# Kernel optimization log

Hardware: AMD Instinct MI355X
Metric: run time of the kernel (lower is better)

The kernel has to match this reference:

```python
import jax, jax.numpy as jnp
import numpy as np
from jax import lax

N, E, F, H, B = 16384, 262144, 32, 128, 16
DI, DS, DC, DTR = 256, 16, 4, 8   # Mamba: d_inner=expand*H, d_state, d_conv, dt_rank=ceil(H/16)
NS, NC = 512, 8                   # num_stations, num line colors
EPS = 1e-5


def _forward(node_features, edge_index, batch, W_in, b_in, W_g1, b_g1, W_g2, b_g2,
             W_inproj, conv_w, conv_b, W_xproj, W_dt, b_dt, A_log, D_p, W_out,
             gamma, beta, Wc, bc, Wh, bh, Wt, bt, Wp1, bp1, Wp2, bp2, Wd, bd, Ws, bs):
    def gcn(x, W, b):
        # GCNConv with self-loops and symmetric normalization
        loops = jnp.arange(N)
        s = jnp.concatenate([edge_index[0], loops])
        d = jnp.concatenate([edge_index[1], loops])
        deg = jax.ops.segment_sum(jnp.ones(s.shape[0], x.dtype), d, num_segments=N)
        dinv = jnp.where(deg > 0, lax.rsqrt(deg), 0.0)
        xw = x @ W
        msg = xw[s] * (dinv[s] * dinv[d])[:, None]
        return jax.ops.segment_sum(msg, d, num_segments=N) + b

    h = jax.nn.relu(node_features @ W_in + b_in)
    h = jax.nn.relu(gcn(h, W_g1, b_g1))
    h_gnn = jax.nn.relu(gcn(h, W_g2, b_g2))

    # --- Mamba block over the node sequence (batch dim of 1, seq_len = N) ---
    xz = h_gnn @ W_inproj                      # (N, 2*DI)
    x, z = xz[:, :DI], xz[:, DI:]
    xp = jnp.pad(x, ((DC - 1, 0), (0, 0)))     # causal depthwise conv1d
    xc = conv_b + sum(xp[k:k + N] * conv_w[:, k] for k in range(DC))
    x = jax.nn.silu(xc)
    dbl = x @ W_xproj                          # (N, DTR + 2*DS)
    dt = jax.nn.softplus(dbl[:, :DTR] @ W_dt + b_dt)   # (N, DI)
    Bm = dbl[:, DTR:DTR + DS]                  # (N, DS)
    Cm = dbl[:, DTR + DS:]                     # (N, DS)
    A = -jnp.exp(A_log)                        # (DI, DS)
    dA = jnp.exp(dt[:, :, None] * A[None])     # (N, DI, DS)
    dBx = dt[:, :, None] * Bm[:, None, :] * x[:, :, None]

    def step(hst, t):
        dA_t, dBx_t, C_t = t
        hst = dA_t * hst + dBx_t               # (DI, DS)
        return hst, hst @ C_t                  # (DI,)

    _, ys = lax.scan(step, jnp.zeros((DI, DS), x.dtype), (dA, dBx, Cm))
    y = (ys + D_p * x) * jax.nn.silu(z)
    h_mamba = y @ W_out                        # (N, H)

    # residual + LayerNorm
    hh = h_gnn + h_mamba
    mu = hh.mean(-1, keepdims=True)
    var = ((hh - mu) ** 2).mean(-1, keepdims=True)
    h_final = (hh - mu) * lax.rsqrt(var + EPS) * gamma + beta

    # global_mean_pool per graph
    counts = jax.ops.segment_sum(jnp.ones(N, h_final.dtype), batch, num_segments=B)
    ge = jax.ops.segment_sum(h_final, batch, num_segments=B) / jnp.maximum(counts, 1.0)[:, None]

    # critic + all policy heads, concatenated: [1,4,3,NS,NS,NS,NC]
    return jnp.concatenate([ge @ Wc + bc, ge @ Wh + bh, ge @ Wt + bt,
                            ge @ Wp1 + bp1, ge @ Wp2 + bp2, ge @ Wd + bd,
                            ge @ Ws + bs], axis=-1)


def setup_inputs() -> dict:
    key = jax.random.key(0)
    ks = list(jax.random.split(key, 20))
    p = lambda i, shape, s=0.02: jax.random.normal(ks[i], shape, jnp.float32) * s
    return dict(
        node_features=jax.random.normal(ks[0], (N, F), jnp.float32),
        edge_index=jax.random.randint(ks[1], (2, E), 0, N),
        batch=jnp.sort(jax.random.randint(ks[2], (N,), 0, B)),
        W_in=p(3, (F, H)), b_in=jnp.zeros((H,), jnp.float32),
        W_g1=p(4, (H, H)), b_g1=jnp.zeros((H,), jnp.float32),
        W_g2=p(5, (H, H)), b_g2=jnp.zeros((H,), jnp.float32),
        W_inproj=p(6, (H, 2 * DI)),
        conv_w=p(7, (DI, DC)), conv_b=jnp.zeros((DI,), jnp.float32),
        W_xproj=p(8, (DI, DTR + 2 * DS)),
        W_dt=p(9, (DTR, DI)), b_dt=jnp.full((DI,), -4.0, jnp.float32),
        A_log=jnp.log(jnp.broadcast_to(jnp.arange(1.0, DS + 1.0, dtype=jnp.float32), (DI, DS))),
        D_p=jnp.ones((DI,), jnp.float32),
        W_out=p(10, (DI, H)),
        gamma=jnp.ones((H,), jnp.float32), beta=jnp.zeros((H,), jnp.float32),
        Wc=p(11, (H, 1)), bc=jnp.zeros((1,), jnp.float32),
        Wh=p(12, (H, 4)), bh=jnp.zeros((4,), jnp.float32),
        Wt=p(13, (H, 3)), bt=jnp.zeros((3,), jnp.float32),
        Wp1=p(14, (H, NS)), bp1=jnp.zeros((NS,), jnp.float32),
        Wp2=p(15, (H, NS)), bp2=jnp.zeros((NS,), jnp.float32),
        Wd=p(16, (H, NS)), bd=jnp.zeros((NS,), jnp.float32),
        Ws=p(17, (H, NC)), bs=jnp.zeros((NC,), jnp.float32),
    )


def reference(node_features, edge_index, batch, W_in, b_in, W_g1, b_g1, W_g2, b_g2,
              W_inproj, conv_w, conv_b, W_xproj, W_dt, b_dt, A_log, D_p, W_out,
              gamma, beta, Wc, bc, Wh, bh, Wt, bt, Wp1, bp1, Wp2, bp2, Wd, bd, Ws, bs):
    return _forward(node_features, edge_index, batch, W_in, b_in, W_g1, b_g1, W_g2, b_g2,
                    W_inproj, conv_w, conv_b, W_xproj, W_dt, b_dt, A_log, D_p, W_out,
                    gamma, beta, Wc, bc, Wh, bh, Wt, bt, Wp1, bp1, Wp2, bp2, Wd, bd, Ws, bs)
```

## Files before the change

kernel.cpp:

```cpp
#include <hip/hip_runtime.h>
#include <math.h>

#define NN 16384
#define EE 262144
#define FF 32
#define HH 128
#define BB 16
#define DI 256
#define DS 16
#define DC 4
#define DTR 8
#define OUTW 1552
#define NCH 256
#define CHLEN 64

__device__ __forceinline__ float siluf(float v) { return v / (1.f + __expf(-v)); }
__device__ __forceinline__ float softplusf(float v) {
    return fmaxf(v, 0.f) + __logf(1.f + __expf(-fabsf(v)));
}

__global__ void zero_kernel(int* __restrict__ cnt, float* __restrict__ ge,
                            int* __restrict__ counts) {
    int idx = blockIdx.x * blockDim.x + threadIdx.x;
    if (idx < NN) cnt[idx] = 0;
    if (idx < BB * HH) ge[idx] = 0.f;
    if (idx < BB) counts[idx] = 0;
}

__global__ void deg_kernel(const int* __restrict__ dst, int* __restrict__ cnt) {
    int e = blockIdx.x * blockDim.x + threadIdx.x;
    if (e < EE) atomicAdd(&cnt[dst[e]], 1);
}

__global__ __launch_bounds__(1024) void prefix_kernel(const int* __restrict__ cnt,
                                                      int* __restrict__ rowptr,
                                                      int* __restrict__ cursor,
                                                      float* __restrict__ dinv) {
    __shared__ int part[1024];
    int tid = threadIdx.x;
    int4 c4[4];
#pragma unroll
    for (int j = 0; j < 4; j++) c4[j] = ((const int4*)cnt)[tid * 4 + j];
    int v[16] = {c4[0].x, c4[0].y, c4[0].z, c4[0].w, c4[1].x, c4[1].y, c4[1].z, c4[1].w,
                 c4[2].x, c4[2].y, c4[2].z, c4[2].w, c4[3].x, c4[3].y, c4[3].z, c4[3].w};
    int s = 0;
#pragma unroll
    for (int j = 0; j < 16; j++) s += v[j];
    part[tid] = s;
    __syncthreads();
    for (int off = 1; off < 1024; off <<= 1) {
        int t = (tid >= off) ? part[tid - off] : 0;
        __syncthreads();
        part[tid] += t;
        __syncthreads();
    }
    int running = part[tid] - s;
    int rp[16];
    float dv[16];
#pragma unroll
    for (int j = 0; j < 16; j++) {
        rp[j] = running;
        running += v[j];
        dv[j] = rsqrtf((float)(v[j] + 1));
    }
#pragma unroll
    for (int j = 0; j < 4; j++) {
        int4 r4; r4.x = rp[j*4]; r4.y = rp[j*4+1]; r4.z = rp[j*4+2]; r4.w = rp[j*4+3];
        ((int4*)rowptr)[tid * 4 + j] = r4;
        ((int4*)cursor)[tid * 4 + j] = r4;
        float4 d4; d4.x = dv[j*4]; d4.y = dv[j*4+1]; d4.z = dv[j*4+2]; d4.w = dv[j*4+3];
        ((float4*)dinv)[tid * 4 + j] = d4;
    }
    if (tid == 1023) rowptr[NN] = part[1023];
}

__global__ void scatter_kernel(const int* __restrict__ src, const int* __restrict__ dst,
                               int* __restrict__ cursor, int* __restrict__ col) {
    int e = blockIdx.x * blockDim.x + threadIdx.x;
    if (e < EE) {
        int d = dst[e];
        int pos = atomicAdd(&cursor[d], 1);
        col[pos] = src[e];
    }
}

__global__ __launch_bounds__(256) void gemm_k(const float* __restrict__ A,
                                              const float* __restrict__ B,
                                              const float* __restrict__ bias,
                                              float* __restrict__ C,
                                              int M, int Nn, int K, int act) {
    __shared__ float As[16][68];
    __shared__ float Bs[16][68];
    int tid = threadIdx.x;
    int m0 = blockIdx.y * 64;
    int n0 = blockIdx.x * 64;
    int ty = tid >> 4, tx = tid & 15;
    float acc[4][4] = {{0.f}};
    for (int k0 = 0; k0 < K; k0 += 16) {
#pragma unroll
        for (int l = 0; l < 4; l++) {
            int idx = tid + l * 256;
            int i = idx >> 4, j = idx & 15;
            As[j][i] = A[(size_t)(m0 + i) * K + k0 + j];
        }
#pragma unroll
        for (int l = 0; l < 4; l++) {
            int idx = tid + l * 256;
            int i = idx >> 6, j = idx & 63;
            int n = n0 + j;
            Bs[i][j] = (n < Nn) ? B[(size_t)(k0 + i) * Nn + n] : 0.f;
        }
        __syncthreads();
#pragma unroll
        for (int kk = 0; kk < 16; kk++) {
            float4 a4 = *(const float4*)&As[kk][ty * 4];
            float4 b4 = *(const float4*)&Bs[kk][tx * 4];
            float av[4] = {a4.x, a4.y, a4.z, a4.w};
            float bv[4] = {b4.x, b4.y, b4.z, b4.w};
#pragma unroll
            for (int r = 0; r < 4; r++)
#pragma unroll
                for (int c = 0; c < 4; c++) acc[r][c] = fmaf(av[r], bv[c], acc[r][c]);
        }
        __syncthreads();
    }
    int nb = n0 + tx * 4;
    if (nb < Nn) {
        float4 bi4 = {0.f, 0.f, 0.f, 0.f};
        if (bias) bi4 = *(const float4*)&bias[nb];
#pragma unroll
        for (int r = 0; r < 4; r++) {
            int m = m0 + ty * 4 + r;
            float4 v;
            v.x = acc[r][0] + bi4.x; v.y = acc[r][1] + bi4.y;
            v.z = acc[r][2] + bi4.z; v.w = acc[r][3] + bi4.w;
            if (act == 1) {
                v.x = fmaxf(v.x, 0.f); v.y = fmaxf(v.y, 0.f);
                v.z = fmaxf(v.z, 0.f); v.w = fmaxf(v.w, 0.f);
            }
            *(float4*)&C[(size_t)m * Nn + nb] = v;
        }
    }
}

union SMemIn {
    struct { float Ns[64][33]; float Ws[32][132]; } s1;
    float Bs[16][68];
};

__global__ __launch_bounds__(256) void gemm_in_g1(const float* __restrict__ nf,
                                                  const float* __restrict__ W_in,
                                                  const float* __restrict__ b_in,
                                                  const float* __restrict__ W_g1,
                                                  float* __restrict__ out) {
    __shared__ SMemIn sm;
    __shared__ float Hs[128][68];
    int tid = threadIdx.x;
    int m0 = blockIdx.y * 64;
    int n0 = blockIdx.x * 64;
    int ty = tid >> 4, tx = tid & 15;
#pragma unroll
    for (int l = 0; l < 2; l++) {
        int q = tid + l * 256;
        int r = q >> 3, c4 = (q & 7) * 4;
        *(float4*)&sm.s1.Ns[r][c4] = *(const float4*)&nf[(size_t)(m0 + r) * FF + c4];
    }
#pragma unroll
    for (int l = 0; l < 4; l++) {
        int q = tid + l * 256;
        int r = q >> 5, c4 = (q & 31) * 4;
        *(float4*)&sm.s1.Ws[r][c4] = *(const float4*)&W_in[(size_t)r * HH + c4];
    }
    __syncthreads();
    {
        float4 b0 = *(const float4*)&b_in[tx * 4];
        float4 b1 = *(const float4*)&b_in[64 + tx * 4];
        float hacc[4][8];
#pragma unroll
        for (int r = 0; r < 4; r++) {
            hacc[r][0] = b0.x; hacc[r][1] = b0.y; hacc[r][2] = b0.z; hacc[r][3] = b0.w;
            hacc[r][4] = b1.x; hacc[r][5] = b1.y; hacc[r][6] = b1.z; hacc[r][7] = b1.w;
        }
#pragma unroll
        for (int k = 0; k < FF; k++) {
            float av[4];
#pragma unroll
            for (int r = 0; r < 4; r++) av[r] = sm.s1.Ns[ty * 4 + r][k];
            float wv[8];
#pragma unroll
            for (int c = 0; c < 4; c++) {
                wv[c]     = sm.s1.Ws[k][tx * 4 + c];
                wv[c + 4] = sm.s1.Ws[k][64 + tx * 4 + c];
            }
#pragma unroll
            for (int r = 0; r < 4; r++)
#pragma unroll
                for (int c = 0; c < 8; c++) hacc[r][c] = fmaf(av[r], wv[c], hacc[r][c]);
        }
#pragma unroll
        for (int r = 0; r < 4; r++)
#pragma unroll
            for (int c = 0; c < 4; c++) {
                Hs[tx * 4 + c][ty * 4 + r]      = fmaxf(hacc[r][c], 0.f);
                Hs[64 + tx * 4 + c][ty * 4 + r] = fmaxf(hacc[r][c + 4], 0.f);
            }
    }
    __syncthreads();
    float acc[4][4] = {{0.f}};
    for (int k0 = 0; k0 < HH; k0 += 16) {
        *(float4*)&sm.Bs[tid >> 4][(tid & 15) * 4] =
            *(const float4*)&W_g1[(size_t)(k0 + (tid >> 4)) * HH + n0 + (tid & 15) * 4];
        __syncthreads();
#pragma unroll
        for (int kk = 0; kk < 16; kk++) {
            float4 a4 = *(const float4*)&Hs[k0 + kk][ty * 4];
            float4 b4 = *(const float4*)&sm.Bs[kk][tx * 4];
            float av[4] = {a4.x, a4.y, a4.z, a4.w};
            float bv[4] = {b4.x, b4.y, b4.z, b4.w};
#pragma unroll
            for (int r = 0; r < 4; r++)
#pragma unroll
                for (int c = 0; c < 4; c++) acc[r][c] = fmaf(av[r], bv[c], acc[r][c]);
        }
        __syncthreads();
    }
#pragma unroll
    for (int r = 0; r < 4; r++) {
        int m = m0 + ty * 4 + r;
        float4 v;
        v.x = acc[r][0]; v.y = acc[r][1]; v.z = acc[r][2]; v.w = acc[r][3];
        *(float4*)&out[(size_t)m * HH + n0 + tx * 4] = v;
    }
}

__global__ __launch_bounds__(512, 4) void gemm_big512_t(const float* __restrict__ A,
                                                        const float* __restrict__ B,
                                                        float* __restrict__ CT,
                                                        int M, int Nn, int K) {
    __shared__ float As[16][132];
    __shared__ float Bs[16][132];
    int tid = threadIdx.x;
    int m0 = blockIdx.y * 128;
    int n0 = blockIdx.x * 128;
    int ty = tid >> 4;
    int tx = tid & 15;
    float acc[4][8] = {{0.f}};
    for (int k0 = 0; k0 < K; k0 += 16) {
        {
            int m = tid >> 2;
            int kc = (tid & 3) * 4;
            float4 a = *(const float4*)&A[(size_t)(m0 + m) * K + k0 + kc];
            As[kc + 0][m] = a.x; As[kc + 1][m] = a.y;
            As[kc + 2][m] = a.z; As[kc + 3][m] = a.w;
        }
        {
            int krow = tid >> 5;
            int c4 = (tid & 31) * 4;
            *(float4*)&Bs[krow][c4] = *(const float4*)&B[(size_t)(k0 + krow) * Nn + n0 + c4];
        }
        __syncthreads();
#pragma unroll
        for (int kk = 0; kk < 16; kk++) {
            float4 a4 = *(const float4*)&As[kk][ty * 4];
            float4 b0 = *(const float4*)&Bs[kk][tx * 4];
            float4 b1 = *(const float4*)&Bs[kk][64 + tx * 4];
            float av[4] = {a4.x, a4.y, a4.z, a4.w};
            float bv[8] = {b0.x, b0.y, b0.z, b0.w, b1.x, b1.y, b1.z, b1.w};
#pragma unroll
            for (int r = 0; r < 4; r++)
#pragma unroll
                for (int c = 0; c < 8; c++) acc[r][c] = fmaf(av[r], bv[c], acc[r][c]);
        }
        __syncthreads();
    }
#pragma unroll
    for (int cc = 0; cc < 4; cc++) {
        float4 v;
        v.x = acc[0][cc]; v.y = acc[1][cc]; v.z = acc[2][cc]; v.w = acc[3][cc];
        *(float4*)&CT[(size_t)(n0 + tx * 4 + cc) * NN + m0 + ty * 4] = v;
        float4 u;
        u.x = acc[0][cc + 4]; u.y = acc[1][cc + 4]; u.z = acc[2][cc + 4]; u.w = acc[3][cc + 4];
        *(float4*)&CT[(size_t)(n0 + 64 + tx * 4 + cc) * NN + m0 + ty * 4] = u;
    }
}

__global__ __launch_bounds__(256) void gemm_xz_dblt(const float* __restrict__ xzt,
                                                    const float* __restrict__ B,
                                                    const float* __restrict__ cw,
                                                    const float* __restrict__ cb,
                                                    float* __restrict__ xst,
                                                    float* __restrict__ dblt) {
    __shared__ float As[16][68];
    __shared__ float Bs[16][68];
    __shared__ float Raw[16][72];
    __shared__ float Ct[64][41];
    int tid = threadIdx.x;
    int m0 = blockIdx.x * 64;
    int ty = tid >> 4, tx = tid & 15;
    float acc[4][4] = {{0.f}};
    for (int k0 = 0; k0 < DI; k0 += 16) {
#pragma unroll
        for (int l = 0; l < 2; l++) {
            int idx = tid + l * 256;
            if (idx < 272) {
                int kk = idx / 17, j = idx % 17;
                int tcol = m0 - 4 + j * 4;
                float4 v;
                if (tcol >= 0) v = *(const float4*)&xzt[(size_t)(k0 + kk) * NN + tcol];
                else { v.x = 0.f; v.y = 0.f; v.z = 0.f; v.w = 0.f; }
                *(float4*)&Raw[kk][j * 4] = v;
            }
        }
#pragma unroll
        for (int l = 0; l < 4; l++) {
            int idx = tid + l * 256;
            int i2 = idx >> 6, j2 = idx & 63;
            Bs[i2][j2] = (j2 < 40) ? B[(size_t)(k0 + i2) * 40 + j2] : 0.f;
        }
        __syncthreads();
#pragma unroll
        for (int l = 0; l < 4; l++) {
            int kk = (tid >> 6) + l * 4;
            int i = tid & 63;
            int d = k0 + kk;
            float w0 = cw[d * DC + 0], w1 = cw[d * DC + 1];
            float w2 = cw[d * DC + 2], w3 = cw[d * DC + 3];
            float v = siluf(cb[d] + w0 * Raw[kk][i + 1] + w1 * Raw[kk][i + 2]
                                  + w2 * Raw[kk][i + 3] + w3 * Raw[kk][i + 4]);
            As[kk][i] = v;
            xst[(size_t)d * NN + m0 + i] = v;
        }
        __syncthreads();
#pragma unroll
        for (int kk = 0; kk < 16; kk++) {
            float4 a4 = *(const float4*)&As[kk][ty * 4];
            float4 b4 = *(const float4*)&Bs[kk][tx * 4];
            float av[4] = {a4.x, a4.y, a4.z, a4.w};
            float bv[4] = {b4.x, b4.y, b4.z, b4.w};
#pragma unroll
            for (int r = 0; r < 4; r++)
#pragma unroll
                for (int c = 0; c < 4; c++) acc[r][c] = fmaf(av[r], bv[c], acc[r][c]);
        }
        __syncthreads();
    }
    if (tx * 4 < 40) {
#pragma unroll
        for (int r = 0; r < 4; r++) {
            int m = ty * 4 + r;
            Ct[m][tx * 4 + 0] = acc[r][0];
            Ct[m][tx * 4 + 1] = acc[r][1];
            Ct[m][tx * 4 + 2] = acc[r][2];
            Ct[m][tx * 4 + 3] = acc[r][3];
        }
    }
    __syncthreads();
#pragma unroll
    for (int l = 0; l < 10; l++) {
        int idx = tid + l * 256;
        int n = idx >> 6, m = idx & 63;
        dblt[(size_t)n * NN + m0 + m] = Ct[m][n];
    }
}

__global__ __launch_bounds__(256) void gemm_at_ln_pool(const float* __restrict__ AT,
                                                       const float* __restrict__ B,
                                                       const float* __restrict__ hg,
                                                       const float* __restrict__ gamma,
                                                       const float* __restrict__ beta,
                                                       const int* __restrict__ batch,
                                                       float* __restrict__ ge,
                                                       int* __restrict__ counts) {
    __shared__ float As[16][36];
    __shared__ float Bs[16][132];
    __shared__ float lnb[32][132];
    __shared__ int gb[32];
    int tid = threadIdx.x;
    int m0 = blockIdx.x * 32;
    int ty = tid >> 4, tx = tid & 15;
    float acc[2][8] = {{0.f}};
    for (int k0 = 0; k0 < 256; k0 += 16) {
        {
            int idx = tid * 2;
            int kk = idx >> 5, i = idx & 31;
            As[kk][i] = AT[(size_t)(k0 + kk) * NN + m0 + i];
            As[kk][i + 1] = AT[(size_t)(k0 + kk) * NN + m0 + i + 1];
        }
        {
            int krow = tid >> 4;
            int c8 = (tid & 15) * 8;
            const float* bp = &B[(size_t)(k0 + krow) * HH + c8];
            *(float4*)&Bs[krow][c8] = *(const float4*)bp;
            *(float4*)&Bs[krow][c8 + 4] = *(const float4*)(bp + 4);
        }
        __syncthreads();
#pragma unroll
        for (int kk = 0; kk < 16; kk++) {
            float a0 = As[kk][ty * 2];
            float a1 = As[kk][ty * 2 + 1];
            float4 b0 = *(const float4*)&Bs[kk][tx * 4];
            float4 b1 = *(const float4*)&Bs[kk][64 + tx * 4];
            float bv[8] = {b0.x, b0.y, b0.z, b0.w, b1.x, b1.y, b1.z, b1.w};
#pragma unroll
            for (int c = 0; c < 8; c++) {
                acc[0][c] = fmaf(a0, bv[c], acc[0][c]);
                acc[1][c] = fmaf(a1, bv[c], acc[1][c]);
            }
        }
        __syncthreads();
    }
    if (tid < 32) gb[tid] = batch[m0 + tid];
    float4 g0 = *(const float4*)&gamma[tx * 4];
    float4 g1 = *(const float4*)&gamma[64 + tx * 4];
    float4 be0 = *(const float4*)&beta[tx * 4];
    float4 be1 = *(const float4*)&beta[64 + tx * 4];
    float gv[8] = {g0.x, g0.y, g0.z, g0.w, g1.x, g1.y, g1.z, g1.w};
    float bv[8] = {be0.x, be0.y, be0.z, be0.w, be1.x, be1.y, be1.z, be1.w};
#pragma unroll
    for (int r = 0; r < 2; r++) {
        int m = m0 + ty * 2 + r;
        float4 h0 = *(const float4*)&hg[(size_t)m * HH + tx * 4];
        float4 h1 = *(const float4*)&hg[(size_t)m * HH + 64 + tx * 4];
        float v[8] = {acc[r][0] + h0.x, acc[r][1] + h0.y, acc[r][2] + h0.z, acc[r][3] + h0.w,
                      acc[r][4] + h1.x, acc[r][5] + h1.y, acc[r][6] + h1.z, acc[r][7] + h1.w};
        float sum = 0.f;
#pragma unroll
        for (int c = 0; c < 8; c++) sum += v[c];
        sum += __shfl_xor(sum, 1); sum += __shfl_xor(sum, 2);
        sum += __shfl_xor(sum, 4); sum += __shfl_xor(sum, 8);
        float mu = sum * (1.f / 128.f);
        float vs = 0.f;
#pragma unroll
        for (int c = 0; c < 8; c++) { float dd = v[c] - mu; vs += dd * dd; }
        vs += __shfl_xor(vs, 1); vs += __shfl_xor(vs, 2);
        vs += __shfl_xor(vs, 4); vs += __shfl_xor(vs, 8);
        float inv = rsqrtf(vs * (1.f / 128.f) + 1e-5f);
        int lr = ty * 2 + r;
        float4 o0, o1;
        o0.x = (v[0] - mu) * inv * gv[0] + bv[0];
        o0.y = (v[1] - mu) * inv * gv[1] + bv[1];
        o0.z = (v[2] - mu) * inv * gv[2] + bv[2];
        o0.w = (v[3] - mu) * inv * gv[3] + bv[3];
        o1.x = (v[4] - mu) * inv * gv[4] + bv[4];
        o1.y = (v[5] - mu) * inv * gv[5] + bv[5];
        o1.z = (v[6] - mu) * inv * gv[6] + bv[6];
        o1.w = (v[7] - mu) * inv * gv[7] + bv[7];
        *(float4*)&lnb[lr][tx * 4] = o0;
        *(float4*)&lnb[lr][64 + tx * 4] = o1;
    }
    __syncthreads();
    if (tid < HH) {
        int f = tid;
        int gcur = gb[0];
        float acc2 = 0.f;
        int cnt = 0;
#pragma unroll 4
        for (int i = 0; i < 32; i++) {
            int g = gb[i];
            if (g != gcur) {
                atomicAdd(&ge[gcur * HH + f], acc2);
                if (f == 0) atomicAdd(&counts[gcur], cnt);
                acc2 = 0.f; cnt = 0; gcur = g;
            }
            acc2 += lnb[i][f];
            cnt++;
        }
        atomicAdd(&ge[gcur * HH + f], acc2);
        if (f == 0) atomicAdd(&counts[gcur], cnt);
    }
}

__global__ __launch_bounds__(256) void gcn_gather4(const float* __restrict__ xw,
                                                   const int* __restrict__ rowptr,
                                                   const int* __restrict__ col,
                                                   const float* __restrict__ dinv,
                                                   const float* __restrict__ b,
                                                   float* __restrict__ out) {
    int tid = threadIdx.x;
    int sub = tid & 31;
    int n = blockIdx.x * 8 + (tid >> 5);
    float dn = dinv[n];
    const float4* xw4 = (const float4*)xw;
    float4 a = xw4[(size_t)n * 32 + sub];
    float ws = dn * dn;
    float4 acc;
    acc.x = a.x * ws; acc.y = a.y * ws; acc.z = a.z * ws; acc.w = a.w * ws;
    int beg = rowptr[n], end = rowptr[n + 1];
    int e = beg;
    for (; e + 4 <= end; e += 4) {
        int s0 = col[e], s1 = col[e + 1], s2 = col[e + 2], s3 = col[e + 3];
        float w0 = dinv[s0] * dn, w1 = dinv[s1] * dn;
        float w2 = dinv[s2] * dn, w3 = dinv[s3] * dn;
        float4 v0 = xw4[(size_t)s0 * 32 + sub];
        float4 v1 = xw4[(size_t)s1 * 32 + sub];
        float4 v2 = xw4[(size_t)s2 * 32 + sub];
        float4 v3 = xw4[(size_t)s3 * 32 + sub];
        acc.x = fmaf(v0.x, w0, acc.x); acc.y = fmaf(v0.y, w0, acc.y);
        acc.z = fmaf(v0.z, w0, acc.z); acc.w = fmaf(v0.w, w0, acc.w);
        acc.x = fmaf(v1.x, w1, acc.x); acc.y = fmaf(v1.y, w1, acc.y);
        acc.z = fmaf(v1.z, w1, acc.z); acc.w = fmaf(v1.w, w1, acc.w);
        acc.x = fmaf(v2.x, w2, acc.x); acc.y = fmaf(v2.y, w2, acc.y);
        acc.z = fmaf(v2.z, w2, acc.z); acc.w = fmaf(v2.w, w2, acc.w);
        acc.x = fmaf(v3.x, w3, acc.x); acc.y = fmaf(v3.y, w3, acc.y);
        acc.z = fmaf(v3.z, w3, acc.z); acc.w = fmaf(v3.w, w3, acc.w);
    }
    for (; e < end; e++) {
        int s0 = col[e];
        float w0 = dinv[s0] * dn;
        float4 v0 = xw4[(size_t)s0 * 32 + sub];
        acc.x = fmaf(v0.x, w0, acc.x); acc.y = fmaf(v0.y, w0, acc.y);
        acc.z = fmaf(v0.z, w0, acc.z); acc.w = fmaf(v0.w, w0, acc.w);
    }
    float4 b4 = ((const float4*)b)[sub];
    acc.x = fmaxf(acc.x + b4.x, 0.f);
    acc.y = fmaxf(acc.y + b4.y, 0.f);
    acc.z = fmaxf(acc.z + b4.z, 0.f);
    acc.w = fmaxf(acc.w + b4.w, 0.f);
    ((float4*)out)[(size_t)n * 32 + sub] = acc;
}

__global__ __launch_bounds__(256, 6) void scan_phase1(const float* __restrict__ xst,
                                                      const float* __restrict__ dblt,
                                                      const float* __restrict__ A_log,
                                                      const float* __restrict__ W_dt,
                                                      const float* __restrict__ b_dt,
                                                      float* __restrict__ chkP,
                                                      float* __restrict__ chkH) {
    __shared__ float Td[32][68];
    __shared__ float Tx[32][68];
    __shared__ float Bs[16][68];
    __shared__ float D8[8][68];
    int tid = threadIdx.x;
    int wave = tid >> 6, lane = tid & 63;
    int sg = lane & 7, dl = lane >> 3;
    int dblk = blockIdx.x, chunk = blockIdx.y;
    int t0 = chunk * CHLEN;
    int dloc = wave * 8 + dl;
    int d = dblk * 32 + dloc;
    int s0 = 2 * sg;
#pragma unroll
    for (int p = 0; p < 2; p++) {
        int linear = tid + p * 256;
        int row = linear >> 4, c4 = (linear & 15) * 4;
        *(float4*)&Tx[row][c4] = *(const float4*)&xst[(size_t)(dblk * 32 + row) * NN + t0 + c4];
    }
    if (tid < 128) {
        int r = tid >> 4, c4 = (tid & 15) * 4;
        *(float4*)&D8[r][c4] = *(const float4*)&dblt[(size_t)r * NN + t0 + c4];
    }
    {
        int s = tid >> 4, c4 = (tid & 15) * 4;
        *(float4*)&Bs[s][c4] = *(const float4*)&dblt[(size_t)(8 + s) * NN + t0 + c4];
    }
    float A0 = -expf(A_log[d * DS + s0]);
    float A1 = -expf(A_log[d * DS + s0 + 1]);
    __syncthreads();
    {
        int row = tid >> 3;
        int tb = (tid & 7) * 8;
        int dd = dblk * 32 + row;
        float bd = b_dt[dd];
        float wv[8];
#pragma unroll
        for (int j = 0; j < 8; j++) wv[j] = W_dt[j * DI + dd];
#pragma unroll
        for (int j = 0; j < 8; j++) {
            int t = tb + j;
            float acc = bd;
#pragma unroll
            for (int k = 0; k < 8; k++) acc = fmaf(D8[k][t], wv[k], acc);
            Td[row][t] = softplusf(acc);
        }
    }
    __syncthreads();
    float h0 = 0.f, h1 = 0.f, P0 = 1.f, P1 = 1.f;
    for (int i = 0; i < CHLEN; i += 4) {
        float4 d4 = *(const float4*)&Td[dloc][i];
        float4 x4 = *(const float4*)&Tx[dloc][i];
        float4 b04 = *(const float4*)&Bs[s0][i];
        float4 b14 = *(const float4*)&Bs[s0 + 1][i];
#define P1S(U) { float dtv = d4.U; float a0 = __expf(dtv * A0); float a1 = __expf(dtv * A1); \
        float dx = dtv * x4.U; h0 = fmaf(a0, h0, dx * b04.U); h1 = fmaf(a1, h1, dx * b14.U); \
        P0 *= a0; P1 *= a1; }
        P1S(x) P1S(y) P1S(z) P1S(w)
#undef P1S
    }
    int idx = chunk * 4096 + d * DS + s0;
    float2 vP; vP.x = P0; vP.y = P1;
    float2 vH; vH.x = h0; vH.y = h1;
    *(float2*)(chkP + idx) = vP;
    *(float2*)(chkH + idx) = vH;
}

__global__ void scan_phase2(const float* __restrict__ chkP, const float* __restrict__ chkH,
                            float* __restrict__ init) {
    int idx = blockIdx.x * blockDim.x + threadIdx.x;
    float h = 0.f;
    for (int c0 = 0; c0 < NCH; c0 += 8) {
        float p[8], q[8];
#pragma unroll
        for (int j = 0; j < 8; j++) {
            p[j] = chkP[(c0 + j) * 4096 + idx];
            q[j] = chkH[(c0 + j) * 4096 + idx];
        }
#pragma unroll
        for (int j = 0; j < 8; j++) {
            init[(c0 + j) * 4096 + idx] = h;
            h = fmaf(p[j], h, q[j]);
        }
    }
}

__global__ __launch_bounds__(256, 6) void scan_phase3(const float* __restrict__ xst,
                                                      const float* __restrict__ dblt,
                                                      const float* __restrict__ A_log,
                                                      const float* __restrict__ W_dt,
                                                      const float* __restrict__ b_dt,
                                                      const float* __restrict__ init,
                                                      const float* __restrict__ D_p,
                                                      const float* __restrict__ xzt,
                                                      float* __restrict__ yt) {
    __shared__ float Td[32][68];
    __shared__ float Tx[32][68];
    __shared__ float Bs[16][68];
    __shared__ float CsD8[16][68];
    int tid = threadIdx.x;
    int wave = tid >> 6, lane = tid & 63;
    int sg = lane & 7, dl = lane >> 3;
    int dblk = blockIdx.x, chunk = blockIdx.y;
    int t0 = chunk * CHLEN;
    int dloc = wave * 8 + dl;
    int d = dblk * 32 + dloc;
    int s0 = 2 * sg;
#pragma unroll
    for (int p = 0; p < 2; p++) {
        int linear = tid + p * 256;
        int row = linear >> 4, c4 = (linear & 15) * 4;
        *(float4*)&Tx[row][c4] = *(const float4*)&xst[(size_t)(dblk * 32 + row) * NN + t0 + c4];
    }
    if (tid < 128) {
        int r = tid >> 4, c4 = (tid & 15) * 4;
        *(float4*)&CsD8[r][c4] = *(const float4*)&dblt[(size_t)r * NN + t0 + c4];
    }
    {
        int s = tid >> 4, c4 = (tid & 15) * 4;
        *(float4*)&Bs[s][c4] = *(const float4*)&dblt[(size_t)(8 + s) * NN + t0 + c4];
    }
    float A0 = -expf(A_log[d * DS + s0]);
    float A1 = -expf(A_log[d * DS + s0 + 1]);
    float Dd = D_p[d];
    float2 ini = *(const float2*)(init + chunk * 4096 + d * DS + s0);
    float h0 = ini.x, h1 = ini.y;
    __syncthreads();
    {
        int row = tid >> 3;
        int tb = (tid & 7) * 8;
        int dd = dblk * 32 + row;
        float bd = b_dt[dd];
        float wv[8];
#pragma unroll
        for (int j = 0; j < 8; j++) wv[j] = W_dt[j * DI + dd];
#pragma unroll
        for (int j = 0; j < 8; j++) {
            int t = tb + j;
            float acc = bd;
#pragma unroll
            for (int k = 0; k < 8; k++) acc = fmaf(CsD8[k][t], wv[k], acc);
            Td[row][t] = softplusf(acc);
        }
    }
    __syncthreads();
    {
        int s = tid >> 4, c4 = (tid & 15) * 4;
        *(float4*)&CsD8[s][c4] = *(const float4*)&dblt[(size_t)(24 + s) * NN + t0 + c4];
    }
    float szv[8];
#pragma unroll
    for (int r = 0; r < 8; r++)
        szv[r] = siluf(xzt[(size_t)(256 + dblk * 32 + wave * 8 + r) * NN + t0 + lane]);
    __syncthreads();
    for (int i = 0; i < CHLEN; i += 4) {
        float4 d4 = *(const float4*)&Td[dloc][i];
        float4 x4 = *(const float4*)&Tx[dloc][i];
        float4 b04 = *(const float4*)&Bs[s0][i];
        float4 b14 = *(const float4*)&Bs[s0 + 1][i];
        float4 c04 = *(const float4*)&CsD8[s0][i];
        float4 c14 = *(const float4*)&CsD8[s0 + 1][i];
        float4 yv;
#define P3S(U) { float dtv = d4.U; float a0 = __expf(dtv * A0); float a1 = __expf(dtv * A1); \
        float dx = dtv * x4.U; h0 = fmaf(a0, h0, dx * b04.U); h1 = fmaf(a1, h1, dx * b14.U); \
        float c = fmaf(h1, c14.U, h0 * c04.U); \
        c += __shfl_xor(c, 1); c += __shfl_xor(c, 2); c += __shfl_xor(c, 4); \
        yv.U = c + Dd * x4.U; }
        P3S(x) P3S(y) P3S(z) P3S(w)
#undef P3S
        if (sg == 0) *(float4*)&Td[dloc][i] = yv;
    }
#pragma unroll
    for (int r = 0; r < 8; r++) {
        int row = wave * 8 + r;
        yt[(size_t)(dblk * 32 + row) * NN + t0 + lane] = Td[row][lane] * szv[r];
    }
}

__global__ void heads_kernel(const float* __restrict__ ge, const int* __restrict__ counts,
                             const float* Wc, const float* bc, const float* Wh, const float* bh,
                             const float* Wt, const float* bt, const float* Wp1, const float* bp1,
                             const float* Wp2, const float* bp2, const float* Wd, const float* bd,
                             const float* Ws, const float* bs, float* __restrict__ out) {
    int col = blockIdx.x * blockDim.x + threadIdx.x;
    int b = blockIdx.y;
    if (col >= OUTW) return;
    const float* W; const float* bi; int lc, w;
    if (col < 1)         { W = Wc;  bi = bc;  lc = col;        w = 1; }
    else if (col < 5)    { W = Wh;  bi = bh;  lc = col - 1;    w = 4; }
    else if (col < 8)    { W = Wt;  bi = bt;  lc = col - 5;    w = 3; }
    else if (col < 520)  { W = Wp1; bi = bp1; lc = col - 8;    w = 512; }
    else if (col < 1032) { W = Wp2; bi = bp2; lc = col - 520;  w = 512; }
    else if (col < 1544) { W = Wd;  bi = bd;  lc = col - 1032; w = 512; }
    else                 { W = Ws;  bi = bs;  lc = col - 1544; w = 8; }
    float scale = 1.f / fmaxf((float)counts[b], 1.f);
    float dot = 0.f;
#pragma unroll 8
    for (int f = 0; f < HH; f++) dot = fmaf(ge[b * HH + f], W[f * w + lc], dot);
    out[(size_t)b * OUTW + col] = bi[lc] + scale * dot;
}

extern "C" void kernel_launch(void* const* d_in, const int* in_sizes, int n_in,
                              void* d_out, int out_size, void* d_ws, size_t ws_size,
                              hipStream_t stream) {
    const float* nf      = (const float*)d_in[0];
    const int*   ei      = (const int*)d_in[1];
    const int*   batch   = (const int*)d_in[2];
    const float* W_in    = (const float*)d_in[3];
    const float* b_in    = (const float*)d_in[4];
    const float* W_g1    = (const float*)d_in[5];
    const float* b_g1    = (const float*)d_in[6];
    const float* W_g2    = (const float*)d_in[7];
    const float* b_g2    = (const float*)d_in[8];
    const float* W_inproj= (const float*)d_in[9];
    const float* conv_w  = (const float*)d_in[10];
    const float* conv_b  = (const float*)d_in[11];
    const float* W_xproj = (const float*)d_in[12];
    const float* W_dt    = (const float*)d_in[13];
    const float* b_dt    = (const float*)d_in[14];
    const float* A_log   = (const float*)d_in[15];
    const float* D_p     = (const float*)d_in[16];
    const float* W_out   = (const float*)d_in[17];
    const float* gamma   = (const float*)d_in[18];
    const float* beta    = (const float*)d_in[19];
    const float* Wc = (const float*)d_in[20]; const float* bc = (const float*)d_in[21];
    const float* Wh = (const float*)d_in[22]; const float* bh = (const float*)d_in[23];
    const float* Wt = (const float*)d_in[24]; const float* bt = (const float*)d_in[25];
    const float* Wp1= (const float*)d_in[26]; const float* bp1= (const float*)d_in[27];
    const float* Wp2= (const float*)d_in[28]; const float* bp2= (const float*)d_in[29];
    const float* Wd = (const float*)d_in[30]; const float* bd = (const float*)d_in[31];
    const float* Ws = (const float*)d_in[32]; const float* bs = (const float*)d_in[33];

    const int* e_src = ei;
    const int* e_dst = ei + EE;

    float* w = (float*)d_ws;
    size_t o = 0;
    float* F0   = w + o; o += (size_t)NN * HH;
    float* F1   = w + o; o += (size_t)NN * HH;
    float* F2   = w + o; o += (size_t)NN * HH;
    float* XZT  = w + o; o += (size_t)NN * 512;
    float* YT   = XZT;
    float* XST  = w + o; o += (size_t)NN * DI;
    float* DBLT = w + o; o += (size_t)NN * 40;
    float* GE   = w + o; o += BB * HH;
    float* DINV = w + o; o += NN;
    int* ip = (int*)(w + o);
    int* CNT    = ip; ip += NN;
    int* ROWPTR = ip; ip += NN + 1;
    int* CURSOR = ip; ip += NN;
    int* COL    = ip; ip += EE;
    int* COUNTS = ip; ip += BB;

    float* CHP  = F0;
    float* CHH  = F0 + (size_t)NCH * 4096;
    float* INI  = F1;

    zero_kernel<<<(NN + 255) / 256, 256, 0, stream>>>(CNT, GE, COUNTS);

    deg_kernel<<<EE / 256, 256, 0, stream>>>(e_dst, CNT);
    prefix_kernel<<<1, 1024, 0, stream>>>(CNT, ROWPTR, CURSOR, DINV);
    scatter_kernel<<<EE / 256, 256, 0, stream>>>(e_src, e_dst, CURSOR, COL);

    gemm_in_g1<<<dim3(2, NN / 64), 256, 0, stream>>>(nf, W_in, b_in, W_g1, F1);
    gcn_gather4<<<NN / 8, 256, 0, stream>>>(F1, ROWPTR, COL, DINV, b_g1, F0);
    gemm_k<<<dim3(2, NN / 64), 256, 0, stream>>>(F0, W_g2, nullptr, F1, NN, HH, HH, 0);
    gcn_gather4<<<NN / 8, 256, 0, stream>>>(F1, ROWPTR, COL, DINV, b_g2, F2);

    gemm_big512_t<<<dim3(4, NN / 128), 512, 0, stream>>>(F2, W_inproj, XZT, NN, 512, HH);
    gemm_xz_dblt<<<NN / 64, 256, 0, stream>>>(XZT, W_xproj, conv_w, conv_b, XST, DBLT);

    scan_phase1<<<dim3(8, NCH), 256, 0, stream>>>(XST, DBLT, A_log, W_dt, b_dt, CHP, CHH);
    scan_phase2<<<16, 256, 0, stream>>>(CHP, CHH, INI);
    scan_phase3<<<dim3(8, NCH), 256, 0, stream>>>(XST, DBLT, A_log, W_dt, b_dt, INI, D_p, XZT, YT);

    gemm_at_ln_pool<<<NN / 32, 256, 0, stream>>>(YT, W_out, F2, gamma, beta, batch, GE, COUNTS);

    heads_kernel<<<dim3((OUTW + 127) / 128, BB), 128, 0, stream>>>(
        GE, COUNTS, Wc, bc, Wh, bh, Wt, bt, Wp1, bp1, Wp2, bp2, Wd, bd, Ws, bs, (float*)d_out);
}
```

Baseline: 399.6 us.

## Remap chunked selective scan to one thread per channel with all states in registers

The chunked Mamba scan kernels are reorganized so each thread owns one inner channel and keeps all 16 state values in registers. Each block now covers all 256 channels for a shorter 32-step chunk, with inputs transposed into padded shared memory. This removes the cross-lane shuffle reduction for the C projection and the separate dt staging pass. The chunk count doubles, so the serial carry pass in phase 2 gets twice as long; it now prefetches the next group of chunk values and reuses buffers in place. The trade-offs are fewer, fatter blocks with higher register pressure.

```diff
diff --git a/kernel.cpp b/kernel.cpp
--- a/kernel.cpp
+++ b/kernel.cpp
@@ -11,8 +11,8 @@
 #define DC 4
 #define DTR 8
 #define OUTW 1552
-#define NCH 256
-#define CHLEN 64
+#define NCH 512
+#define CHLEN 32
 
 __device__ __forceinline__ float siluf(float v) { return v / (1.f + __expf(-v)); }
 __device__ __forceinline__ float softplusf(float v) {
@@ -519,187 +519,197 @@
     ((float4*)out)[(size_t)n * 32 + sub] = acc;
 }
 
-__global__ __launch_bounds__(256, 6) void scan_phase1(const float* __restrict__ xst,
-                                                      const float* __restrict__ dblt,
-                                                      const float* __restrict__ A_log,
-                                                      const float* __restrict__ W_dt,
-                                                      const float* __restrict__ b_dt,
-                                                      float* __restrict__ chkP,
-                                                      float* __restrict__ chkH) {
-    __shared__ float Td[32][68];
-    __shared__ float Tx[32][68];
-    __shared__ float Bs[16][68];
-    __shared__ float D8[8][68];
+__global__ __launch_bounds__(256) void scan_phase1(const float* __restrict__ xst,
+                                                   const float* __restrict__ dblt,
+                                                   const float* __restrict__ A_log,
+                                                   const float* __restrict__ W_dt,
+                                                   const float* __restrict__ b_dt,
+                                                   float* __restrict__ chkP,
+                                                   float* __restrict__ chkH) {
+    __shared__ float Tx[CHLEN][257];
+    __shared__ float D8s[8][33];
+    __shared__ float Bt[CHLEN][20];
     int tid = threadIdx.x;
-    int wave = tid >> 6, lane = tid & 63;
-    int sg = lane & 7, dl = lane >> 3;
-    int dblk = blockIdx.x, chunk = blockIdx.y;
+    int chunk = blockIdx.x;
     int t0 = chunk * CHLEN;
-    int dloc = wave * 8 + dl;
-    int d = dblk * 32 + dloc;
-    int s0 = 2 * sg;
-#pragma unroll
-    for (int p = 0; p < 2; p++) {
-        int linear = tid + p * 256;
-        int row = linear >> 4, c4 = (linear & 15) * 4;
-        *(float4*)&Tx[row][c4] = *(const float4*)&xst[(size_t)(dblk * 32 + row) * NN + t0 + c4];
-    }
-    if (tid < 128) {
-        int r = tid >> 4, c4 = (tid & 15) * 4;
-        *(float4*)&D8[r][c4] = *(const float4*)&dblt[(size_t)r * NN + t0 + c4];
+#pragma unroll
+    for (int jj = 0; jj < 32; jj++) {
+        int lin = tid + jj * 256;
+        int dd = lin >> 5, t = lin & 31;
+        Tx[t][dd] = xst[(size_t)dd * NN + t0 + t];
     }
     {
-        int s = tid >> 4, c4 = (tid & 15) * 4;
-        *(float4*)&Bs[s][c4] = *(const float4*)&dblt[(size_t)(8 + s) * NN + t0 + c4];
-    }
-    float A0 = -expf(A_log[d * DS + s0]);
-    float A1 = -expf(A_log[d * DS + s0 + 1]);
+        int s = tid >> 5, t = tid & 31;
+        D8s[s][t] = dblt[(size_t)s * NN + t0 + t];
+    }
+#pragma unroll
+    for (int jj = 0; jj < 2; jj++) {
+        int lin = tid + jj * 256;
+        int s = lin >> 5, t = lin & 31;
+        Bt[t][s] = dblt[(size_t)(8 + s) * NN + t0 + t];
+    }
+    int d = tid;
+    float wv[8];
+#pragma unroll
+    for (int k = 0; k < 8; k++) wv[k] = W_dt[k * DI + d];
+    float bd = b_dt[d];
+    float A[16];
+#pragma unroll
+    for (int q = 0; q < 4; q++) {
+        float4 al = *(const float4*)&A_log[d * DS + q * 4];
+        A[q*4+0] = -expf(al.x); A[q*4+1] = -expf(al.y);
+        A[q*4+2] = -expf(al.z); A[q*4+3] = -expf(al.w);
+    }
+    float h[16], P[16];
+#pragma unroll
+    for (int s = 0; s < 16; s++) { h[s] = 0.f; P[s] = 1.f; }
     __syncthreads();
-    {
-        int row = tid >> 3;
-        int tb = (tid & 7) * 8;
-        int dd = dblk * 32 + row;
-        float bd = b_dt[dd];
-        float wv[8];
-#pragma unroll
-        for (int j = 0; j < 8; j++) wv[j] = W_dt[j * DI + dd];
-#pragma unroll
-        for (int j = 0; j < 8; j++) {
-            int t = tb + j;
-            float acc = bd;
-#pragma unroll
-            for (int k = 0; k < 8; k++) acc = fmaf(D8[k][t], wv[k], acc);
-            Td[row][t] = softplusf(acc);
-        }
-    }
-    __syncthreads();
-    float h0 = 0.f, h1 = 0.f, P0 = 1.f, P1 = 1.f;
-    for (int i = 0; i < CHLEN; i += 4) {
-        float4 d4 = *(const float4*)&Td[dloc][i];
-        float4 x4 = *(const float4*)&Tx[dloc][i];
-        float4 b04 = *(const float4*)&Bs[s0][i];
-        float4 b14 = *(const float4*)&Bs[s0 + 1][i];
-#define P1S(U) { float dtv = d4.U; float a0 = __expf(dtv * A0); float a1 = __expf(dtv * A1); \
-        float dx = dtv * x4.U; h0 = fmaf(a0, h0, dx * b04.U); h1 = fmaf(a1, h1, dx * b14.U); \
-        P0 *= a0; P1 *= a1; }
-        P1S(x) P1S(y) P1S(z) P1S(w)
-#undef P1S
-    }
-    int idx = chunk * 4096 + d * DS + s0;
-    float2 vP; vP.x = P0; vP.y = P1;
-    float2 vH; vH.x = h0; vH.y = h1;
-    *(float2*)(chkP + idx) = vP;
-    *(float2*)(chkH + idx) = vH;
-}
-
-__global__ void scan_phase2(const float* __restrict__ chkP, const float* __restrict__ chkH,
-                            float* __restrict__ init) {
+    for (int t = 0; t < CHLEN; t++) {
+        float acc = bd;
+#pragma unroll
+        for (int k = 0; k < 8; k++) acc = fmaf(D8s[k][t], wv[k], acc);
+        float dtv = softplusf(acc);
+        float dx = dtv * Tx[t][d];
+        float4 b0 = *(const float4*)&Bt[t][0];
+        float4 b1 = *(const float4*)&Bt[t][4];
+        float4 b2 = *(const float4*)&Bt[t][8];
+        float4 b3 = *(const float4*)&Bt[t][12];
+        float Bv[16] = {b0.x,b0.y,b0.z,b0.w, b1.x,b1.y,b1.z,b1.w,
+                        b2.x,b2.y,b2.z,b2.w, b3.x,b3.y,b3.z,b3.w};
+#pragma unroll
+        for (int s = 0; s < 16; s++) {
+            float a = __expf(dtv * A[s]);
+            h[s] = fmaf(a, h[s], dx * Bv[s]);
+            P[s] *= a;
+        }
+    }
+    size_t base = (size_t)chunk * 4096 + d * 16;
+#pragma unroll
+    for (int q = 0; q < 4; q++) {
+        float4 vP; vP.x = P[q*4]; vP.y = P[q*4+1]; vP.z = P[q*4+2]; vP.w = P[q*4+3];
+        float4 vH; vH.x = h[q*4]; vH.y = h[q*4+1]; vH.z = h[q*4+2]; vH.w = h[q*4+3];
+        *(float4*)&chkP[base + q*4] = vP;
+        *(float4*)&chkH[base + q*4] = vH;
+    }
+}
+
+__global__ void scan_phase2(const float* chkP, const float* chkH, float* init) {
     int idx = blockIdx.x * blockDim.x + threadIdx.x;
     float h = 0.f;
+    float p[8], q[8], pn[8], qn[8];
+#pragma unroll
+    for (int j = 0; j < 8; j++) {
+        p[j] = chkP[j * 4096 + idx];
+        q[j] = chkH[j * 4096 + idx];
+    }
     for (int c0 = 0; c0 < NCH; c0 += 8) {
-        float p[8], q[8];
-#pragma unroll
-        for (int j = 0; j < 8; j++) {
-            p[j] = chkP[(c0 + j) * 4096 + idx];
-            q[j] = chkH[(c0 + j) * 4096 + idx];
+        if (c0 + 8 < NCH) {
+#pragma unroll
+            for (int j = 0; j < 8; j++) {
+                pn[j] = chkP[(c0 + 8 + j) * 4096 + idx];
+                qn[j] = chkH[(c0 + 8 + j) * 4096 + idx];
+            }
         }
 #pragma unroll
         for (int j = 0; j < 8; j++) {
             init[(c0 + j) * 4096 + idx] = h;
             h = fmaf(p[j], h, q[j]);
         }
-    }
-}
-
-__global__ __launch_bounds__(256, 6) void scan_phase3(const float* __restrict__ xst,
-                                                      const float* __restrict__ dblt,
-                                                      const float* __restrict__ A_log,
-                                                      const float* __restrict__ W_dt,
-                                                      const float* __restrict__ b_dt,
-                                                      const float* __restrict__ init,
-                                                      const float* __restrict__ D_p,
-                                                      const float* __restrict__ xzt,
-                                                      float* __restrict__ yt) {
-    __shared__ float Td[32][68];
-    __shared__ float Tx[32][68];
-    __shared__ float Bs[16][68];
-    __shared__ float CsD8[16][68];
+#pragma unroll
+        for (int j = 0; j < 8; j++) { p[j] = pn[j]; q[j] = qn[j]; }
+    }
+}
+
+__global__ __launch_bounds__(256) void scan_phase3(const float* __restrict__ xst,
+                                                   const float* __restrict__ dblt,
+                                                   const float* __restrict__ A_log,
+                                                   const float* __restrict__ W_dt,
+                                                   const float* __restrict__ b_dt,
+                                                   const float* __restrict__ init,
+                                                   const float* __restrict__ D_p,
+                                                   const float* __restrict__ xzt,
+                                                   float* __restrict__ yt) {
+    __shared__ float Tx[CHLEN][257];
+    __shared__ float Yl[CHLEN][257];
+    __shared__ float D8s[8][33];
+    __shared__ float Bt[CHLEN][20];
+    __shared__ float Ctt[CHLEN][20];
     int tid = threadIdx.x;
-    int wave = tid >> 6, lane = tid & 63;
-    int sg = lane & 7, dl = lane >> 3;
-    int dblk = blockIdx.x, chunk = blockIdx.y;
+    int chunk = blockIdx.x;
     int t0 = chunk * CHLEN;
-    int dloc = wave * 8 + dl;
-    int d = dblk * 32 + dloc;
-    int s0 = 2 * sg;
-#pragma unroll
-    for (int p = 0; p < 2; p++) {
-        int linear = tid + p * 256;
-        int row = linear >> 4, c4 = (linear & 15) * 4;
-        *(float4*)&Tx[row][c4] = *(const float4*)&xst[(size_t)(dblk * 32 + row) * NN + t0 + c4];
-    }
-    if (tid < 128) {
-        int r = tid >> 4, c4 = (tid & 15) * 4;
-        *(float4*)&CsD8[r][c4] = *(const float4*)&dblt[(size_t)r * NN + t0 + c4];
+#pragma unroll
+    for (int jj = 0; jj < 32; jj++) {
+        int lin = tid + jj * 256;
+        int dd = lin >> 5, t = lin & 31;
+        Tx[t][dd] = xst[(size_t)dd * NN + t0 + t];
     }
     {
-        int s = tid >> 4, c4 = (tid & 15) * 4;
-        *(float4*)&Bs[s][c4] = *(const float4*)&dblt[(size_t)(8 + s) * NN + t0 + c4];
-    }
-    float A0 = -expf(A_log[d * DS + s0]);
-    float A1 = -expf(A_log[d * DS + s0 + 1]);
+        int s = tid >> 5, t = tid & 31;
+        D8s[s][t] = dblt[(size_t)s * NN + t0 + t];
+    }
+#pragma unroll
+    for (int jj = 0; jj < 2; jj++) {
+        int lin = tid + jj * 256;
+        int s = lin >> 5, t = lin & 31;
+        Bt[t][s]  = dblt[(size_t)(8 + s) * NN + t0 + t];
+        Ctt[t][s] = dblt[(size_t)(24 + s) * NN + t0 + t];
+    }
+    int d = tid;
+    float wv[8];
+#pragma unroll
+    for (int k = 0; k < 8; k++) wv[k] = W_dt[k * DI + d];
+    float bd = b_dt[d];
     float Dd = D_p[d];
-    float2 ini = *(const float2*)(init + chunk * 4096 + d * DS + s0);
-    float h0 = ini.x, h1 = ini.y;
+    float A[16];
+#pragma unroll
+    for (int q = 0; q < 4; q++) {
+        float4 al = *(const float4*)&A_log[d * DS + q * 4];
+        A[q*4+0] = -expf(al.x); A[q*4+1] = -expf(al.y);
+        A[q*4+2] = -expf(al.z); A[q*4+3] = -expf(al.w);
+    }
+    float h[16];
+    size_t base = (size_t)chunk * 4096 + d * 16;
+#pragma unroll
+    for (int q = 0; q < 4; q++) {
+        float4 vi = *(const float4*)&init[base + q * 4];
+        h[q*4+0] = vi.x; h[q*4+1] = vi.y; h[q*4+2] = vi.z; h[q*4+3] = vi.w;
+    }
     __syncthreads();
-    {
-        int row = tid >> 3;
-        int tb = (tid & 7) * 8;
-        int dd = dblk * 32 + row;
-        float bd = b_dt[dd];
-        float wv[8];
-#pragma unroll
-        for (int j = 0; j < 8; j++) wv[j] = W_dt[j * DI + dd];
-#pragma unroll
-        for (int j = 0; j < 8; j++) {
-            int t = tb + j;
-            float acc = bd;
-#pragma unroll
-            for (int k = 0; k < 8; k++) acc = fmaf(CsD8[k][t], wv[k], acc);
-            Td[row][t] = softplusf(acc);
-        }
+    for (int t = 0; t < CHLEN; t++) {
+        float acc = bd;
+#pragma unroll
+        for (int k = 0; k < 8; k++) acc = fmaf(D8s[k][t], wv[k], acc);
+        float dtv = softplusf(acc);
+        float x = Tx[t][d];
+        float dx = dtv * x;
+        float4 b0 = *(const float4*)&Bt[t][0];
+        float4 b1 = *(const float4*)&Bt[t][4];
+        float4 b2 = *(const float4*)&Bt[t][8];
+        float4 b3 = *(const float4*)&Bt[t][12];
+        float4 c0 = *(const float4*)&Ctt[t][0];
+        float4 c1 = *(const float4*)&Ctt[t][4];
+        float4 c2 = *(const float4*)&Ctt[t][8];
+        float4 c3 = *(const float4*)&Ctt[t][12];
+        float Bv[16] = {b0.x,b0.y,b0.z,b0.w, b1.x,b1.y,b1.z,b1.w,
+                        b2.x,b2.y,b2.z,b2.w, b3.x,b3.y,b3.z,b3.w};
+        float Cv[16] = {c0.x,c0.y,c0.z,c0.w, c1.x,c1.y,c1.z,c1.w,
+                        c2.x,c2.y,c2.z,c2.w, c3.x,c3.y,c3.z,c3.w};
+        float y = 0.f;
+#pragma unroll
+        for (int s = 0; s < 16; s++) {
+            float a = __expf(dtv * A[s]);
+            h[s] = fmaf(a, h[s], dx * Bv[s]);
+            y = fmaf(h[s], Cv[s], y);
+        }
+        Yl[t][d] = fmaf(Dd, x, y);
     }
     __syncthreads();
-    {
-        int s = tid >> 4, c4 = (tid & 15) * 4;
-        *(float4*)&CsD8[s][c4] = *(const float4*)&dblt[(size_t)(24 + s) * NN + t0 + c4];
-    }
-    float szv[8];
-#pragma unroll
-    for (int r = 0; r < 8; r++)
-        szv[r] = siluf(xzt[(size_t)(256 + dblk * 32 + wave * 8 + r) * NN + t0 + lane]);
-    __syncthreads();
-    for (int i = 0; i < CHLEN; i += 4) {
-        float4 d4 = *(const float4*)&Td[dloc][i];
-        float4 x4 = *(const float4*)&Tx[dloc][i];
-        float4 b04 = *(const float4*)&Bs[s0][i];
-        float4 b14 = *(const float4*)&Bs[s0 + 1][i];
-        float4 c04 = *(const float4*)&CsD8[s0][i];
-        float4 c14 = *(const float4*)&CsD8[s0 + 1][i];
-        float4 yv;
-#define P3S(U) { float dtv = d4.U; float a0 = __expf(dtv * A0); float a1 = __expf(dtv * A1); \
-        float dx = dtv * x4.U; h0 = fmaf(a0, h0, dx * b04.U); h1 = fmaf(a1, h1, dx * b14.U); \
-        float c = fmaf(h1, c14.U, h0 * c04.U); \
-        c += __shfl_xor(c, 1); c += __shfl_xor(c, 2); c += __shfl_xor(c, 4); \
-        yv.U = c + Dd * x4.U; }
-        P3S(x) P3S(y) P3S(z) P3S(w)
-#undef P3S
-        if (sg == 0) *(float4*)&Td[dloc][i] = yv;
-    }
-#pragma unroll
-    for (int r = 0; r < 8; r++) {
-        int row = wave * 8 + r;
-        yt[(size_t)(dblk * 32 + row) * NN + t0 + lane] = Td[row][lane] * szv[r];
+#pragma unroll
+    for (int jj = 0; jj < 32; jj++) {
+        int lin = tid + jj * 256;
+        int dd = lin >> 5, t = lin & 31;
+        float z = xzt[(size_t)(256 + dd) * NN + t0 + t];
+        yt[(size_t)dd * NN + t0 + t] = Yl[t][dd] * siluf(z);
     }
 }
 
@@ -779,8 +789,8 @@
     int* COUNTS = ip; ip += BB;
 
     float* CHP  = F0;
-    float* CHH  = F0 + (size_t)NCH * 4096;
-    float* INI  = F1;
+    float* CHH  = F1;
+    float* INI  = CHP;
 
     zero_kernel<<<(NN + 255) / 256, 256, 0, stream>>>(CNT, GE, COUNTS);
 
@@ -796,9 +806,9 @@
     gemm_big512_t<<<dim3(4, NN / 128), 512, 0, stream>>>(F2, W_inproj, XZT, NN, 512, HH);
     gemm_xz_dblt<<<NN / 64, 256, 0, stream>>>(XZT, W_xproj, conv_w, conv_b, XST, DBLT);
 
-    scan_phase1<<<dim3(8, NCH), 256, 0, stream>>>(XST, DBLT, A_log, W_dt, b_dt, CHP, CHH);
+    scan_phase1<<<NCH, 256, 0, stream>>>(XST, DBLT, A_log, W_dt, b_dt, CHP, CHH);
     scan_phase2<<<16, 256, 0, stream>>>(CHP, CHH, INI);
-    scan_phase3<<<dim3(8, NCH), 256, 0, stream>>>(XST, DBLT, A_log, W_dt, b_dt, INI, D_p, XZT, YT);
+    scan_phase3<<<NCH, 256, 0, stream>>>(XST, DBLT, A_log, W_dt, b_dt, INI, D_p, XZT, YT);
 
     gemm_at_ln_pool<<<NN / 32, 256, 0, stream>>>(YT, W_out, F2, gamma, beta, batch, GE, COUNTS);
 
```

Result: slower. 418.9 us (+4.8%).
